# Kernel optimization log

Measured on AMD Instinct MI355X. Metric: run time of the kernel, lower is better.

Reference implementation:

```python
import jax, jax.numpy as jnp
import numpy as np

EMBED_DIM = 1024
N_HEADS = 16
HEAD_DIM = EMBED_DIM // N_HEADS
B, S = 4, 2048


def _rope_tables(seq_len, dim):
    inv_freq = 1.0 / (10000.0 ** (jnp.arange(0, dim, 2, dtype=jnp.float32) / dim))
    freqs = jnp.arange(seq_len, dtype=jnp.float32)[:, None] * inv_freq[None, :]  # [S, dim/2]
    return jnp.cos(freqs), jnp.sin(freqs)


def _apply_rope(x, cos, sin):
    # x: [B, H, S, D]; interleaved-pair complex rotation
    x2 = x.reshape(*x.shape[:-1], HEAD_DIM // 2, 2)
    x0, x1 = x2[..., 0], x2[..., 1]
    c = cos[None, None, :, :]
    s = sin[None, None, :, :]
    r0 = x0 * c - x1 * s
    r1 = x0 * s + x1 * c
    return jnp.stack([r0, r1], axis=-1).reshape(x.shape)


def setup_inputs() -> dict:
    key = jax.random.key(0)
    ks = jax.random.split(key, 8)
    sc = 0.02
    return {
        "query": jax.random.normal(ks[0], (B, S, EMBED_DIM), jnp.float32),
        "key": jax.random.normal(ks[1], (B, S, EMBED_DIM), jnp.float32),
        "value": jax.random.normal(ks[2], (B, S, EMBED_DIM), jnp.float32),
        "Wq": jax.random.normal(ks[3], (EMBED_DIM, EMBED_DIM), jnp.float32) * sc,
        "Wk": jax.random.normal(ks[4], (EMBED_DIM, EMBED_DIM), jnp.float32) * sc,
        "Wv": jax.random.normal(ks[5], (EMBED_DIM, EMBED_DIM), jnp.float32) * sc,
        "Wo": jax.random.normal(ks[6], (EMBED_DIM, EMBED_DIM), jnp.float32) * sc,
        "bo": jnp.zeros((EMBED_DIM,), jnp.float32),
    }


def reference(query, key, value, Wq, Wk, Wv, Wo, bo):
    b, s, _ = query.shape
    # torch nn.Linear: y = x @ W.T
    Q = (query @ Wq.T).reshape(b, s, N_HEADS, HEAD_DIM).transpose(0, 2, 1, 3)
    K = (key @ Wk.T).reshape(b, s, N_HEADS, HEAD_DIM).transpose(0, 2, 1, 3)
    V = (value @ Wv.T).reshape(b, s, N_HEADS, HEAD_DIM).transpose(0, 2, 1, 3)
    cos, sin = _rope_tables(s, HEAD_DIM)
    Q = _apply_rope(Q, cos, sin)
    K = _apply_rope(K, cos, sin)
    scores = jnp.einsum("bhqd,bhkd->bhqk", Q, K) / jnp.sqrt(jnp.float32(HEAD_DIM))
    attn = jax.nn.softmax(scores, axis=-1)
    out = jnp.einsum("bhqk,bhkd->bhqd", attn, V)
    out = out.transpose(0, 2, 1, 3).reshape(b, s, EMBED_DIM)
    return out @ Wo.T + bo
```

## Files before the change

### kernel.cpp

```cpp
#include <hip/hip_runtime.h>
#include <math.h>

typedef __attribute__((ext_vector_type(4))) float f32x4;
typedef __attribute__((ext_vector_type(16))) float f32x16;
typedef __attribute__((ext_vector_type(8))) __bf16 bf16x8;
typedef __attribute__((ext_vector_type(4))) unsigned int u32x4;
typedef __attribute__((ext_vector_type(4))) unsigned short u16x4;

#define DEVI __device__ __forceinline__

constexpr size_t WS_WB  = 0;
constexpr size_t WS_COS = 4ull * 1024 * 1024 * 2;
constexpr size_t WS_SIN = WS_COS + 2048 * 32 * 4;
constexpr size_t WS_QH  = WS_SIN + 2048 * 32 * 4;
constexpr size_t WS_KH  = WS_QH + 64ull * 2048 * 64 * 2;
constexpr size_t WS_VT  = WS_KH + 64ull * 2048 * 64 * 2;
constexpr size_t WS_AO  = WS_VT + 64ull * 64 * 2048 * 2;

DEVI unsigned short f2bf(float x) {
  union { float f; unsigned int u; } v; v.f = x;
  unsigned int r = v.u + 0x7fffu + ((v.u >> 16) & 1u);
  return (unsigned short)(r >> 16);
}

DEVI unsigned cvtpk(float a, float b) {
  union { __bf16 h[2]; unsigned u; } x;
  x.h[0] = (__bf16)a; x.h[1] = (__bf16)b;
  return x.u;
}

DEVI void ld_lds16(const void* g, void* l) {
  __builtin_amdgcn_global_load_lds((const __attribute__((address_space(1))) void*)g,
                                   (__attribute__((address_space(3))) void*)l, 16, 0, 0);
}

__global__ __launch_bounds__(256) void cvt_w(const float* __restrict__ w0,
                                             const float* __restrict__ w1,
                                             const float* __restrict__ w2,
                                             const float* __restrict__ w3,
                                             unsigned short* __restrict__ out) {
  const float* w = blockIdx.y == 0 ? w0 : blockIdx.y == 1 ? w1 : blockIdx.y == 2 ? w2 : w3;
  int i = (blockIdx.x * 256 + threadIdx.x) * 4;
  f32x4 v = *(const f32x4*)(w + i);
  u16x4 o;
  o.x = f2bf(v.x); o.y = f2bf(v.y); o.z = f2bf(v.z); o.w = f2bf(v.w);
  *(u16x4*)(out + (size_t)blockIdx.y * 1048576 + i) = o;
}

__global__ __launch_bounds__(256) void rope_tab(float* __restrict__ cosT,
                                                float* __restrict__ sinT) {
  int idx = blockIdx.x * 256 + threadIdx.x;
  int s = idx >> 5, i = idx & 31;
  double ang = (double)s * pow(10000.0, -(double)i / 32.0);
  cosT[idx] = (float)cos(ang);
  sinT[idx] = (float)sin(ang);
}

__global__ __launch_bounds__(256) void gemm_qkv(const float* __restrict__ Aq,
                                                const float* __restrict__ Ak,
                                                const float* __restrict__ Av,
                                                const unsigned short* __restrict__ Wb,
                                                unsigned short* __restrict__ Qh,
                                                unsigned short* __restrict__ Kh,
                                                unsigned short* __restrict__ Vt,
                                                const float* __restrict__ cosT,
                                                const float* __restrict__ sinT) {
  __shared__ __align__(16) float AsF[128 * 32];
  __shared__ __align__(16) unsigned short Bs[128 * 32];

  const int mat = blockIdx.y;
  const float* A = mat == 0 ? Aq : mat == 1 ? Ak : Av;
  const unsigned short* W = Wb + (size_t)mat * 1048576;

  const int tid = threadIdx.x;
  const int lane = tid & 63;
  const int wave = tid >> 6;
  const int flat = blockIdx.x;
  const int wgid = (flat & 7) * 64 + (flat >> 3);
  const int m0 = (wgid >> 3) * 128;
  const int n0 = (wgid & 7) * 128;
  const int wm = (wave >> 1) * 64;
  const int wn = (wave & 1) * 64;
  const int hi2 = lane >> 4;

  f32x4 acc[4][4] = {};

  for (int kt = 0; kt < 32; ++kt) {
    const int k0 = kt * 32;
#pragma unroll
    for (int i = 0; i < 4; ++i) {
      int g = i * 256 + tid;
      int row = g >> 3, u = g & 7;
      ld_lds16(A + (size_t)(m0 + row) * 1024 + k0 + ((u ^ (row & 7)) << 2),
               AsF + ((i * 256 + wave * 64) << 2));
    }
#pragma unroll
    for (int i = 0; i < 2; ++i) {
      int g = i * 256 + tid;
      int row = g >> 2, u = g & 3;
      ld_lds16(W + (size_t)(n0 + row) * 1024 + k0 + ((u ^ ((row >> 1) & 3)) << 3),
               Bs + ((i * 256 + wave * 64) << 3));
    }
    __syncthreads();

    bf16x8 af[4], bfr[4];
#pragma unroll
    for (int x = 0; x < 4; ++x) {
      int row = wm + x * 16 + (lane & 15);
      int swz = row & 7;
      f32x4 a0 = *(const f32x4*)(AsF + row * 32 + (((hi2 * 2) ^ swz) << 2));
      f32x4 a1 = *(const f32x4*)(AsF + row * 32 + (((hi2 * 2 + 1) ^ swz) << 2));
      union { u32x4 u; bf16x8 v; } f;
      f.u.x = cvtpk(a0.x, a0.y); f.u.y = cvtpk(a0.z, a0.w);
      f.u.z = cvtpk(a1.x, a1.y); f.u.w = cvtpk(a1.z, a1.w);
      af[x] = f.v;
      int brow = wn + x * 16 + (lane & 15);
      bfr[x] = *(const bf16x8*)(Bs + brow * 32 + ((hi2 ^ ((brow >> 1) & 3)) << 3));
    }
#pragma unroll
    for (int mi = 0; mi < 4; ++mi)
#pragma unroll
      for (int ni = 0; ni < 4; ++ni)
        acc[mi][ni] = __builtin_amdgcn_mfma_f32_16x16x32_bf16(af[mi], bfr[ni], acc[mi][ni], 0, 0, 0);
    __syncthreads();
  }

  const int b = m0 >> 11;
  const int sbase = (m0 & 2047) + wm + ((lane >> 4) << 2);

  if (mat < 2) {
    unsigned short* dst = mat == 0 ? Qh : Kh;
    const float scale = mat == 0 ? 0.18033688011112042f : 1.0f;
#pragma unroll
    for (int ni = 0; ni < 4; ++ni) {
      int n = n0 + wn + ni * 16 + (lane & 15);
      int h = n >> 6, d = n & 63, fi = d >> 1;
      size_t base = (size_t)(b * 16 + h) * 131072 + d;
#pragma unroll
      for (int mi = 0; mi < 4; ++mi) {
#pragma unroll
        for (int r = 0; r < 4; ++r) {
          int s = sbase + mi * 16 + r;
          float v = acc[mi][ni][r];
          float p = __shfl_xor(v, 1);
          float c = cosT[(s << 5) + fi], sn = sinT[(s << 5) + fi];
          float ov = (d & 1) ? (p * sn + v * c) : (v * c - p * sn);
          dst[base + (size_t)s * 64] = f2bf(ov * scale);
        }
      }
    }
  } else {
#pragma unroll
    for (int ni = 0; ni < 4; ++ni) {
      int n = n0 + wn + ni * 16 + (lane & 15);
      int h = n >> 6, d = n & 63;
#pragma unroll
      for (int mi = 0; mi < 4; ++mi) {
        u16x4 pk;
        pk.x = f2bf(acc[mi][ni][0]); pk.y = f2bf(acc[mi][ni][1]);
        pk.z = f2bf(acc[mi][ni][2]); pk.w = f2bf(acc[mi][ni][3]);
        int s = sbase + mi * 16;
        *(u16x4*)(Vt + ((size_t)(b * 16 + h) * 64 + d) * 2048 + s) = pk;
      }
    }
  }
}

__global__ __launch_bounds__(256) void gemm_wo(const unsigned short* __restrict__ Ab,
                                               const unsigned short* __restrict__ W,
                                               float* __restrict__ outp,
                                               const float* __restrict__ bo) {
  __shared__ __align__(16) unsigned short Asb[128 * 32];
  __shared__ __align__(16) unsigned short Bs[128 * 32];

  const int tid = threadIdx.x;
  const int lane = tid & 63;
  const int wave = tid >> 6;
  const int flat = blockIdx.x;
  const int wgid = (flat & 7) * 64 + (flat >> 3);
  const int m0 = (wgid >> 3) * 128;
  const int n0 = (wgid & 7) * 128;
  const int wm = (wave >> 1) * 64;
  const int wn = (wave & 1) * 64;
  const int hi2 = lane >> 4;

  f32x4 acc[4][4] = {};

  for (int kt = 0; kt < 32; ++kt) {
    const int k0 = kt * 32;
#pragma unroll
    for (int i = 0; i < 2; ++i) {
      int g = i * 256 + tid;
      int row = g >> 2, u = g & 3;
      ld_lds16(Ab + (size_t)(m0 + row) * 1024 + k0 + ((u ^ ((row >> 1) & 3)) << 3),
               Asb + ((i * 256 + wave * 64) << 3));
      ld_lds16(W + (size_t)(n0 + row) * 1024 + k0 + ((u ^ ((row >> 1) & 3)) << 3),
               Bs + ((i * 256 + wave * 64) << 3));
    }
    __syncthreads();

    bf16x8 af[4], bfr[4];
#pragma unroll
    for (int x = 0; x < 4; ++x) {
      int row = wm + x * 16 + (lane & 15);
      af[x] = *(const bf16x8*)(Asb + row * 32 + ((hi2 ^ ((row >> 1) & 3)) << 3));
      int brow = wn + x * 16 + (lane & 15);
      bfr[x] = *(const bf16x8*)(Bs + brow * 32 + ((hi2 ^ ((brow >> 1) & 3)) << 3));
    }
#pragma unroll
    for (int mi = 0; mi < 4; ++mi)
#pragma unroll
      for (int ni = 0; ni < 4; ++ni)
        acc[mi][ni] = __builtin_amdgcn_mfma_f32_16x16x32_bf16(af[mi], bfr[ni], acc[mi][ni], 0, 0, 0);
    __syncthreads();
  }

#pragma unroll
  for (int ni = 0; ni < 4; ++ni) {
    int n = n0 + wn + ni * 16 + (lane & 15);
    float bias = bo[n];
#pragma unroll
    for (int mi = 0; mi < 4; ++mi)
#pragma unroll
      for (int r = 0; r < 4; ++r) {
        int m = m0 + wm + mi * 16 + ((lane >> 4) << 2) + r;
        outp[(size_t)m * 1024 + n] = acc[mi][ni][r] + bias;
      }
  }
}

DEVI float tile_sm(f32x16& s0, f32x16& s1, bf16x8* pa) {
  float a0 = 0.f, a1 = 0.f, a2 = 0.f, a3 = 0.f;
#pragma unroll
  for (int r = 0; r < 16; r += 4) {
    s0[r] = __builtin_amdgcn_exp2f(s0[r]);         a0 += s0[r];
    s0[r + 1] = __builtin_amdgcn_exp2f(s0[r + 1]); a1 += s0[r + 1];
    s0[r + 2] = __builtin_amdgcn_exp2f(s0[r + 2]); a2 += s0[r + 2];
    s0[r + 3] = __builtin_amdgcn_exp2f(s0[r + 3]); a3 += s0[r + 3];
  }
#pragma unroll
  for (int r = 0; r < 16; r += 4) {
    s1[r] = __builtin_amdgcn_exp2f(s1[r]);         a0 += s1[r];
    s1[r + 1] = __builtin_amdgcn_exp2f(s1[r + 1]); a1 += s1[r + 1];
    s1[r + 2] = __builtin_amdgcn_exp2f(s1[r + 2]); a2 += s1[r + 2];
    s1[r + 3] = __builtin_amdgcn_exp2f(s1[r + 3]); a3 += s1[r + 3];
  }
#pragma unroll
  for (int blk = 0; blk < 2; ++blk) {
    const f32x16& s = blk ? s1 : s0;
#pragma unroll
    for (int half = 0; half < 2; ++half) {
      int o = half * 8;
      unsigned u0 = cvtpk(s[o + 0], s[o + 1]);
      unsigned u1 = cvtpk(s[o + 2], s[o + 3]);
      unsigned u2 = cvtpk(s[o + 4], s[o + 5]);
      unsigned u3 = cvtpk(s[o + 6], s[o + 7]);
      auto r02 = __builtin_amdgcn_permlane32_swap(u0, u2, false, false);
      auto r13 = __builtin_amdgcn_permlane32_swap(u1, u3, false, false);
      union { u32x4 u; bf16x8 v; } f;
      f.u.x = r02[0]; f.u.y = r13[0]; f.u.z = r02[1]; f.u.w = r13[1];
      pa[blk * 2 + half] = f.v;
    }
  }
  return (a0 + a1) + (a2 + a3);
}

__global__ __launch_bounds__(256, 2) void attn_kernel(const unsigned short* __restrict__ Qh,
                                                      const unsigned short* __restrict__ Kh,
                                                      const unsigned short* __restrict__ Vt,
                                                      unsigned short* __restrict__ AOb) {
  __shared__ __align__(16) unsigned short SM[4][4096];

  const int tid = threadIdx.x, lane = tid & 63, wave = tid >> 6;
  const int lid = blockIdx.x;
  const int xcd = lid & 7, slot = lid >> 3;
  const int bh = xcd * 8 + (slot >> 3);
  const int qb = slot & 7;
  const int q0 = qb * 256 + wave * 64;
  const int lq = lane & 31, hi = lane >> 5;

  const unsigned short* Qgb = Qh + (size_t)bh * 131072;
  const unsigned short* Kgb = Kh + (size_t)bh * 131072;
  const unsigned short* Vgb = Vt + (size_t)bh * 131072;

  bf16x8 qfa[4], qfb[4];
#pragma unroll
  for (int st = 0; st < 4; ++st) {
    qfa[st] = *(const bf16x8*)(Qgb + (size_t)(q0 + lq) * 64 + st * 16 + hi * 8);
    qfb[st] = *(const bf16x8*)(Qgb + (size_t)(q0 + 32 + lq) * 64 + st * 16 + hi * 8);
  }

  const int r0 = wave * 8 + (lane >> 3);
  const int u0 = lane & 7;
  const int sw = (u0 ^ (r0 & 7)) << 3;
  const unsigned short* kp0 = Kgb + r0 * 64 + sw;
  const unsigned short* kp1 = Kgb + (32 + r0) * 64 + sw;
  const unsigned short* vp0 = Vgb + (size_t)r0 * 2048 + sw;
  const unsigned short* vp1 = Vgb + (size_t)(32 + r0) * 2048 + sw;
  const int d0 = wave * 512, d1 = 2048 + wave * 512;

  auto stage = [&](int buf, int kt) {
    unsigned short* Kd = SM[buf * 2];
    unsigned short* Vd = SM[buf * 2 + 1];
    ld_lds16(kp0 + kt * 4096, Kd + d0);
    ld_lds16(kp1 + kt * 4096, Kd + d1);
    ld_lds16(vp0 + kt * 64, Vd + d0);
    ld_lds16(vp1 + kt * 64, Vd + d1);
  };
  auto frag = [&](const unsigned short* base, int row, int c) -> bf16x8 {
    return *(const bf16x8*)(base + row * 64 + (((c ^ (row & 7)) << 3)));
  };

  f32x16 o0a = {}, o1a = {}, o0b = {}, o1b = {};
  float lsA = 0.f, lsB = 0.f;

  stage(0, 0);

  for (int kt = 0; kt < 32; ++kt) {
    const int cur = kt & 1;
    if (kt < 31) {
      stage(cur ^ 1, kt + 1);
      asm volatile("s_waitcnt vmcnt(4)" ::: "memory");
    } else {
      asm volatile("s_waitcnt vmcnt(0)" ::: "memory");
    }
    __builtin_amdgcn_s_barrier();
    const unsigned short* Kc = SM[cur * 2];
    const unsigned short* Vc = SM[cur * 2 + 1];

    bf16x8 kf0[4], kf1[4], vf0[4], vf1[4];
#pragma unroll
    for (int st = 0; st < 4; ++st) {
      kf0[st] = frag(Kc, lq, st * 2 + hi);
      kf1[st] = frag(Kc, 32 + lq, st * 2 + hi);
      vf0[st] = frag(Vc, lq, st * 2 + hi);
      vf1[st] = frag(Vc, 32 + lq, st * 2 + hi);
    }

    f32x16 s0a = {}, s1a = {}, s0b = {}, s1b = {};
#pragma unroll
    for (int st = 0; st < 4; ++st) {
      s0a = __builtin_amdgcn_mfma_f32_32x32x16_bf16(kf0[st], qfa[st], s0a, 0, 0, 0);
      s1a = __builtin_amdgcn_mfma_f32_32x32x16_bf16(kf1[st], qfa[st], s1a, 0, 0, 0);
      s0b = __builtin_amdgcn_mfma_f32_32x32x16_bf16(kf0[st], qfb[st], s0b, 0, 0, 0);
      s1b = __builtin_amdgcn_mfma_f32_32x32x16_bf16(kf1[st], qfb[st], s1b, 0, 0, 0);
    }

    bf16x8 paA[4], paB[4];
    lsA += tile_sm(s0a, s1a, paA);
    lsB += tile_sm(s0b, s1b, paB);

#pragma unroll
    for (int kc = 0; kc < 4; ++kc) {
      o0a = __builtin_amdgcn_mfma_f32_32x32x16_bf16(paA[kc], vf0[kc], o0a, 0, 0, 0);
      o1a = __builtin_amdgcn_mfma_f32_32x32x16_bf16(paA[kc], vf1[kc], o1a, 0, 0, 0);
      o0b = __builtin_amdgcn_mfma_f32_32x32x16_bf16(paB[kc], vf0[kc], o0b, 0, 0, 0);
      o1b = __builtin_amdgcn_mfma_f32_32x32x16_bf16(paB[kc], vf1[kc], o1b, 0, 0, 0);
    }
  }

  lsA += __shfl_xor(lsA, 32);
  lsB += __shfl_xor(lsB, 32);
  const int b = bh >> 4, h = bh & 15;
#pragma unroll
  for (int r = 0; r < 16; ++r) {
    int row = (r & 3) + 8 * (r >> 2) + 4 * hi;
    float ia = 1.0f / __shfl(lsA, row);
    float ib = 1.0f / __shfl(lsB, row);
    unsigned short* da = AOb + (size_t)(b * 2048 + q0 + row) * 1024 + h * 64;
    unsigned short* db = AOb + (size_t)(b * 2048 + q0 + 32 + row) * 1024 + h * 64;
    da[lq] = f2bf(o0a[r] * ia);
    da[32 + lq] = f2bf(o1a[r] * ia);
    db[lq] = f2bf(o0b[r] * ib);
    db[32 + lq] = f2bf(o1b[r] * ib);
  }
}

extern "C" void kernel_launch(void* const* d_in, const int* in_sizes, int n_in,
                              void* d_out, int out_size, void* d_ws, size_t ws_size,
                              hipStream_t stream) {
  const float* query = (const float*)d_in[0];
  const float* key = (const float*)d_in[1];
  const float* value = (const float*)d_in[2];
  const float* Wq = (const float*)d_in[3];
  const float* Wk = (const float*)d_in[4];
  const float* Wv = (const float*)d_in[5];
  const float* Wo = (const float*)d_in[6];
  const float* bo = (const float*)d_in[7];

  char* ws = (char*)d_ws;
  unsigned short* Wb = (unsigned short*)(ws + WS_WB);
  float* cosT = (float*)(ws + WS_COS);
  float* sinT = (float*)(ws + WS_SIN);
  unsigned short* Qh = (unsigned short*)(ws + WS_QH);
  unsigned short* Kh = (unsigned short*)(ws + WS_KH);
  unsigned short* Vt = (unsigned short*)(ws + WS_VT);
  unsigned short* AOb = (unsigned short*)(ws + WS_AO);

  cvt_w<<<dim3(1024, 4), 256, 0, stream>>>(Wq, Wk, Wv, Wo, Wb);
  rope_tab<<<256, 256, 0, stream>>>(cosT, sinT);
  gemm_qkv<<<dim3(512, 3), 256, 0, stream>>>(query, key, value, Wb, Qh, Kh, Vt, cosT, sinT);
  attn_kernel<<<512, 256, 0, stream>>>(Qh, Kh, Vt, AOb);
  gemm_wo<<<512, 256, 0, stream>>>(AOb, Wb + 3145728, (float*)d_out, bo);
}
```

Baseline: 216.9 us.

## Double attention KV tile to 128 keys and merge weight-convert with rope-table kernel

The attention kernel now stages 128 keys per iteration instead of 64, using 16 outer iterations over a larger 32KB-per-buffer K/V tile with a 16-way swizzle for V. Each staged tile is processed in two 64-key halves, and a trailing barrier now guards buffer reuse. This halves the number of barrier/wait points per key sweep at the cost of more LDS, which may reduce occupancy. Separately, the weight-conversion and rope-table kernels are fused into one launch to remove a kernel launch.

```diff
diff --git a/kernel.cpp b/kernel.cpp
--- a/kernel.cpp
+++ b/kernel.cpp
@@ -34,26 +34,28 @@
                                    (__attribute__((address_space(3))) void*)l, 16, 0, 0);
 }
 
-__global__ __launch_bounds__(256) void cvt_w(const float* __restrict__ w0,
-                                             const float* __restrict__ w1,
-                                             const float* __restrict__ w2,
-                                             const float* __restrict__ w3,
-                                             unsigned short* __restrict__ out) {
+__global__ __launch_bounds__(256) void prep(const float* __restrict__ w0,
+                                            const float* __restrict__ w1,
+                                            const float* __restrict__ w2,
+                                            const float* __restrict__ w3,
+                                            unsigned short* __restrict__ out,
+                                            float* __restrict__ cosT,
+                                            float* __restrict__ sinT) {
+  if (blockIdx.y == 4) {
+    if (blockIdx.x >= 256) return;
+    int idx = blockIdx.x * 256 + threadIdx.x;
+    int s = idx >> 5, i = idx & 31;
+    double ang = (double)s * pow(10000.0, -(double)i / 32.0);
+    cosT[idx] = (float)cos(ang);
+    sinT[idx] = (float)sin(ang);
+    return;
+  }
   const float* w = blockIdx.y == 0 ? w0 : blockIdx.y == 1 ? w1 : blockIdx.y == 2 ? w2 : w3;
   int i = (blockIdx.x * 256 + threadIdx.x) * 4;
   f32x4 v = *(const f32x4*)(w + i);
   u16x4 o;
   o.x = f2bf(v.x); o.y = f2bf(v.y); o.z = f2bf(v.z); o.w = f2bf(v.w);
   *(u16x4*)(out + (size_t)blockIdx.y * 1048576 + i) = o;
-}
-
-__global__ __launch_bounds__(256) void rope_tab(float* __restrict__ cosT,
-                                                float* __restrict__ sinT) {
-  int idx = blockIdx.x * 256 + threadIdx.x;
-  int s = idx >> 5, i = idx & 31;
-  double ang = (double)s * pow(10000.0, -(double)i / 32.0);
-  cosT[idx] = (float)cos(ang);
-  sinT[idx] = (float)sin(ang);
 }
 
 __global__ __launch_bounds__(256) void gemm_qkv(const float* __restrict__ Aq,
@@ -269,7 +271,8 @@
                                                       const unsigned short* __restrict__ Kh,
                                                       const unsigned short* __restrict__ Vt,
                                                       unsigned short* __restrict__ AOb) {
-  __shared__ __align__(16) unsigned short SM[4][4096];
+  __shared__ __align__(16) unsigned short Ks[2][8192];
+  __shared__ __align__(16) unsigned short Vs[2][8192];
 
   const int tid = threadIdx.x, lane = tid & 63, wave = tid >> 6;
   const int lid = blockIdx.x;
@@ -290,25 +293,25 @@
     qfb[st] = *(const bf16x8*)(Qgb + (size_t)(q0 + 32 + lq) * 64 + st * 16 + hi * 8);
   }
 
-  const int r0 = wave * 8 + (lane >> 3);
-  const int u0 = lane & 7;
-  const int sw = (u0 ^ (r0 & 7)) << 3;
-  const unsigned short* kp0 = Kgb + r0 * 64 + sw;
-  const unsigned short* kp1 = Kgb + (32 + r0) * 64 + sw;
-  const unsigned short* vp0 = Vgb + (size_t)r0 * 2048 + sw;
-  const unsigned short* vp1 = Vgb + (size_t)(32 + r0) * 2048 + sw;
-  const int d0 = wave * 512, d1 = 2048 + wave * 512;
-
   auto stage = [&](int buf, int kt) {
-    unsigned short* Kd = SM[buf * 2];
-    unsigned short* Vd = SM[buf * 2 + 1];
-    ld_lds16(kp0 + kt * 4096, Kd + d0);
-    ld_lds16(kp1 + kt * 4096, Kd + d1);
-    ld_lds16(vp0 + kt * 64, Vd + d0);
-    ld_lds16(vp1 + kt * 64, Vd + d1);
+    const int kbase = kt * 128;
+    unsigned short* Kd = Ks[buf];
+    unsigned short* Vd = Vs[buf];
+#pragma unroll
+    for (int i = 0; i < 4; ++i) {
+      int g = i * 256 + tid;
+      int kr = g >> 3, ku = g & 7;
+      int vr = g >> 4, vu = g & 15;
+      int db = (i * 256 + wave * 64) << 3;
+      ld_lds16(Kgb + (size_t)(kbase + kr) * 64 + ((ku ^ (kr & 7)) << 3), Kd + db);
+      ld_lds16(Vgb + (size_t)vr * 2048 + kbase + ((vu ^ (vr & 15)) << 3), Vd + db);
+    }
   };
-  auto frag = [&](const unsigned short* base, int row, int c) -> bf16x8 {
-    return *(const bf16x8*)(base + row * 64 + (((c ^ (row & 7)) << 3)));
+  auto kfrag = [&](const unsigned short* Kc, int row, int c) -> bf16x8 {
+    return *(const bf16x8*)(Kc + row * 64 + ((c ^ (row & 7)) << 3));
+  };
+  auto vfrag = [&](const unsigned short* Vc, int row, int c) -> bf16x8 {
+    return *(const bf16x8*)(Vc + row * 128 + ((c ^ (row & 15)) << 3));
   };
 
   f32x16 o0a = {}, o1a = {}, o0b = {}, o1b = {};
@@ -316,46 +319,53 @@
 
   stage(0, 0);
 
-  for (int kt = 0; kt < 32; ++kt) {
+  for (int kt = 0; kt < 16; ++kt) {
     const int cur = kt & 1;
-    if (kt < 31) {
+    if (kt < 15) {
       stage(cur ^ 1, kt + 1);
-      asm volatile("s_waitcnt vmcnt(4)" ::: "memory");
+      asm volatile("s_waitcnt vmcnt(8)" ::: "memory");
     } else {
       asm volatile("s_waitcnt vmcnt(0)" ::: "memory");
     }
     __builtin_amdgcn_s_barrier();
-    const unsigned short* Kc = SM[cur * 2];
-    const unsigned short* Vc = SM[cur * 2 + 1];
-
-    bf16x8 kf0[4], kf1[4], vf0[4], vf1[4];
-#pragma unroll
-    for (int st = 0; st < 4; ++st) {
-      kf0[st] = frag(Kc, lq, st * 2 + hi);
-      kf1[st] = frag(Kc, 32 + lq, st * 2 + hi);
-      vf0[st] = frag(Vc, lq, st * 2 + hi);
-      vf1[st] = frag(Vc, 32 + lq, st * 2 + hi);
-    }
-
-    f32x16 s0a = {}, s1a = {}, s0b = {}, s1b = {};
-#pragma unroll
-    for (int st = 0; st < 4; ++st) {
-      s0a = __builtin_amdgcn_mfma_f32_32x32x16_bf16(kf0[st], qfa[st], s0a, 0, 0, 0);
-      s1a = __builtin_amdgcn_mfma_f32_32x32x16_bf16(kf1[st], qfa[st], s1a, 0, 0, 0);
-      s0b = __builtin_amdgcn_mfma_f32_32x32x16_bf16(kf0[st], qfb[st], s0b, 0, 0, 0);
-      s1b = __builtin_amdgcn_mfma_f32_32x32x16_bf16(kf1[st], qfb[st], s1b, 0, 0, 0);
-    }
-
-    bf16x8 paA[4], paB[4];
-    lsA += tile_sm(s0a, s1a, paA);
-    lsB += tile_sm(s0b, s1b, paB);
-
-#pragma unroll
-    for (int kc = 0; kc < 4; ++kc) {
-      o0a = __builtin_amdgcn_mfma_f32_32x32x16_bf16(paA[kc], vf0[kc], o0a, 0, 0, 0);
-      o1a = __builtin_amdgcn_mfma_f32_32x32x16_bf16(paA[kc], vf1[kc], o1a, 0, 0, 0);
-      o0b = __builtin_amdgcn_mfma_f32_32x32x16_bf16(paB[kc], vf0[kc], o0b, 0, 0, 0);
-      o1b = __builtin_amdgcn_mfma_f32_32x32x16_bf16(paB[kc], vf1[kc], o1b, 0, 0, 0);
+    const unsigned short* Kc = Ks[cur];
+    const unsigned short* Vc = Vs[cur];
+
+#pragma unroll
+    for (int h = 0; h < 2; ++h) {
+      bf16x8 kf0[4], kf1[4], vf0[4], vf1[4];
+#pragma unroll
+      for (int st = 0; st < 4; ++st) {
+        kf0[st] = kfrag(Kc, h * 64 + lq, st * 2 + hi);
+        kf1[st] = kfrag(Kc, h * 64 + 32 + lq, st * 2 + hi);
+        vf0[st] = vfrag(Vc, lq, h * 8 + st * 2 + hi);
+        vf1[st] = vfrag(Vc, 32 + lq, h * 8 + st * 2 + hi);
+      }
+
+      f32x16 s0a = {}, s1a = {}, s0b = {}, s1b = {};
+#pragma unroll
+      for (int st = 0; st < 4; ++st) {
+        s0a = __builtin_amdgcn_mfma_f32_32x32x16_bf16(kf0[st], qfa[st], s0a, 0, 0, 0);
+        s1a = __builtin_amdgcn_mfma_f32_32x32x16_bf16(kf1[st], qfa[st], s1a, 0, 0, 0);
+        s0b = __builtin_amdgcn_mfma_f32_32x32x16_bf16(kf0[st], qfb[st], s0b, 0, 0, 0);
+        s1b = __builtin_amdgcn_mfma_f32_32x32x16_bf16(kf1[st], qfb[st], s1b, 0, 0, 0);
+      }
+
+      bf16x8 paA[4], paB[4];
+      lsA += tile_sm(s0a, s1a, paA);
+      lsB += tile_sm(s0b, s1b, paB);
+
+#pragma unroll
+      for (int kc = 0; kc < 4; ++kc) {
+        o0a = __builtin_amdgcn_mfma_f32_32x32x16_bf16(paA[kc], vf0[kc], o0a, 0, 0, 0);
+        o1a = __builtin_amdgcn_mfma_f32_32x32x16_bf16(paA[kc], vf1[kc], o1a, 0, 0, 0);
+        o0b = __builtin_amdgcn_mfma_f32_32x32x16_bf16(paB[kc], vf0[kc], o0b, 0, 0, 0);
+        o1b = __builtin_amdgcn_mfma_f32_32x32x16_bf16(paB[kc], vf1[kc], o1b, 0, 0, 0);
+      }
+    }
+
+    if (kt < 15) {
+      __builtin_amdgcn_s_barrier();
     }
   }
 
@@ -397,8 +407,7 @@
   unsigned short* Vt = (unsigned short*)(ws + WS_VT);
   unsigned short* AOb = (unsigned short*)(ws + WS_AO);
 
-  cvt_w<<<dim3(1024, 4), 256, 0, stream>>>(Wq, Wk, Wv, Wo, Wb);
-  rope_tab<<<256, 256, 0, stream>>>(cosT, sinT);
+  prep<<<dim3(1024, 5), 256, 0, stream>>>(Wq, Wk, Wv, Wo, Wb, cosT, sinT);
   gemm_qkv<<<dim3(512, 3), 256, 0, stream>>>(query, key, value, Wb, Qh, Kh, Vt, cosT, sinT);
   attn_kernel<<<512, 256, 0, stream>>>(Qh, Kh, Vt, AOb);
   gemm_wo<<<512, 256, 0, stream>>>(AOb, Wb + 3145728, (float*)d_out, bo);
```

New measurement: 279.7 us. +29.0%, slower.
